# Kernel optimization log

Measured on AMD Instinct MI355X. Metric: run time of the kernel, lower is better.

The kernel has to match this reference:

```python
import jax, jax.numpy as jnp
import numpy as np

D = 1024          # hidden_dim
H = 16            # num_heads
G = 32            # number of graphs in the batch
N = 512           # nodes per graph (equal-size graphs -> the per-graph loop becomes one batched attention)
T = G * N         # total nodes
EPS = 1e-5


def _layernorm(x, g, b):
    mu = jnp.mean(x, axis=-1, keepdims=True)
    var = jnp.mean(jnp.square(x - mu), axis=-1, keepdims=True)
    return (x - mu) * jax.lax.rsqrt(var + EPS) * g + b


def setup_inputs() -> dict:
    key = jax.random.key(0)
    ks = jax.random.split(key, 10)
    s = 0.02
    inp = {
        "h": jax.random.normal(ks[0], (T, D), dtype=jnp.float32),
        "w_in": jax.random.normal(ks[1], (3 * D, D), dtype=jnp.float32) * s,   # MHA in_proj_weight
        "b_in": jnp.zeros((3 * D,), dtype=jnp.float32),
        "w_out": jax.random.normal(ks[2], (D, D), dtype=jnp.float32) * s,      # MHA out_proj
        "b_out": jnp.zeros((D,), dtype=jnp.float32),
        "ln1_g": jnp.ones((D,), dtype=jnp.float32),
        "ln1_b": jnp.zeros((D,), dtype=jnp.float32),
        "ln2_g": jnp.ones((D,), dtype=jnp.float32),
        "ln2_b": jnp.zeros((D,), dtype=jnp.float32),
        "ffn_w1": jax.random.normal(ks[3], (2 * D, D), dtype=jnp.float32) * s,
        "ffn_b1": jnp.zeros((2 * D,), dtype=jnp.float32),
        "ffn_w2": jax.random.normal(ks[4], (D, 2 * D), dtype=jnp.float32) * s,
        "ffn_b2": jnp.zeros((D,), dtype=jnp.float32),
        "edge_index": jax.random.randint(ks[5], (2, 65536), 0, T, dtype=jnp.int64),
        "batch": jnp.repeat(jnp.arange(G, dtype=jnp.int64), N),
        "num_graphs": G,
    }
    return inp


def reference(h, w_in, b_in, w_out, b_out, ln1_g, ln1_b, ln2_g, ln2_b,
              ffn_w1, ffn_b1, ffn_w2, ffn_b2, edge_index, batch, num_graphs):
    # Per-graph self-attention: equal-size contiguous graphs -> reshape to [G, N, D]
    hd = D // H
    x = h.reshape(num_graphs, -1, D)                       # [G, N, D]
    n = x.shape[1]
    qkv = x @ w_in.T + b_in                                # [G, N, 3D]
    q, k, v = jnp.split(qkv, 3, axis=-1)
    q = q.reshape(num_graphs, n, H, hd).transpose(0, 2, 1, 3)  # [G, H, N, hd]
    k = k.reshape(num_graphs, n, H, hd).transpose(0, 2, 1, 3)
    v = v.reshape(num_graphs, n, H, hd).transpose(0, 2, 1, 3)
    scores = jnp.einsum('ghnd,ghmd->ghnm', q, k) / np.sqrt(hd)
    attn = jax.nn.softmax(scores, axis=-1)
    o = jnp.einsum('ghnm,ghmd->ghnd', attn, v)             # [G, H, N, hd]
    o = o.transpose(0, 2, 1, 3).reshape(num_graphs, n, D)
    o = o @ w_out.T + b_out
    x = _layernorm(x + o, ln1_g, ln1_b)                    # residual + norm1
    f = jax.nn.relu(x @ ffn_w1.T + ffn_b1) @ ffn_w2.T + ffn_b2  # dropout: eval mode (identity)
    x = _layernorm(x + f, ln2_g, ln2_b)                    # residual + norm2
    return x.reshape(-1, D)                                # [T, D]
```

## Files before the change

### kernel.cpp

```cpp
#include <hip/hip_runtime.h>
#include <stdint.h>

typedef unsigned short u16;
typedef __attribute__((ext_vector_type(8))) short bf16x8;
typedef __attribute__((ext_vector_type(4))) float f32x4;

#define AS1C(p) ((const __attribute__((address_space(1))) char*)(const char*)(p))
#define AS3C(p) ((__attribute__((address_space(3))) char*)(char*)(p))

static __device__ __forceinline__ u16 f2bf(float f) {
  uint32_t u = __builtin_bit_cast(uint32_t, f);
  u = (u + 0x7FFFu + ((u >> 16) & 1u)) >> 16;
  return (u16)u;
}

__global__ __launch_bounds__(256) void k_f2bf(const float* __restrict__ src,
                                              u16* __restrict__ dst, int n4) {
  int i = blockIdx.x * blockDim.x + threadIdx.x;
  if (i >= n4) return;
  float4 v = reinterpret_cast<const float4*>(src)[i];
  ushort4 o;
  o.x = f2bf(v.x); o.y = f2bf(v.y); o.z = f2bf(v.z); o.w = f2bf(v.w);
  reinterpret_cast<ushort4*>(dst)[i] = o;
}

#define BAR()  do { asm volatile("" ::: "memory"); __builtin_amdgcn_s_barrier(); asm volatile("" ::: "memory"); } while (0)
#define WLG()  asm volatile("s_waitcnt lgkmcnt(0)" ::: "memory")
#define WV4()  asm volatile("s_waitcnt vmcnt(4)" ::: "memory")

template<bool OUT_BF16, bool RELU>
__global__ __launch_bounds__(512, 2) void k_gemm256(const u16* __restrict__ A,
                                                    const u16* __restrict__ B,
                                                    const float* __restrict__ bias,
                                                    void* __restrict__ C,
                                                    int M, int N, int K) {
  __shared__ __align__(16) char lds[131072];
  const int tid = threadIdx.x, lane = tid & 63, wid = tid >> 6;
  const int wm = wid >> 2, wn = wid & 3;

  const int nbx = N >> 8;
  const int cpx = gridDim.x >> 3;
  const int sid = ((int)blockIdx.x & 7) * cpx + ((int)blockIdx.x >> 3);
  const int bm = (sid / nbx) << 8;
  const int bn = (sid % nbx) << 8;

  int ga[2], gb[2];
  unsigned wdst[2];
#pragma unroll
  for (int c = 0; c < 2; ++c) {
    const int o = wid * 2048 + c * 1024 + lane * 16;
    const int r = o >> 7;
    const int kb = (((o >> 4) & 7) ^ (r & 7)) * 16;
    ga[c] = (bm + r) * K * 2 + kb;
    gb[c] = (bn + r) * K * 2 + kb;
    wdst[c] = (unsigned)__builtin_amdgcn_readfirstlane(wid * 2048 + c * 1024);
  }
  const int hStep = 128 * K * 2;
  const char* Ag = (const char*)A;
  const char* Bg = (const char*)B;

  const int rA = (wm * 128 + (lane & 15)) * 128;
  const int rB = 32768 + (wn * 64 + (lane & 15)) * 128;
  int ck[2];
#pragma unroll
  for (int s = 0; s < 2; ++s) ck[s] = ((s * 4 + (lane >> 4)) ^ (lane & 7)) * 16;

  f32x4 acc[8][4];
#pragma unroll
  for (int m = 0; m < 8; ++m)
#pragma unroll
    for (int n = 0; n < 4; ++n) acc[m][n] = 0.f;
  bf16x8 am[4][2], b0f[2][2], b1f[2][2];

#define STG(isB, half, t, buf) do { \
  _Pragma("unroll") for (int c_ = 0; c_ < 2; ++c_) { \
    const char* s_ = ((isB) ? Bg : Ag) + ((isB) ? gb[c_] : ga[c_]) + (half) * hStep + (t) * 128; \
    __builtin_amdgcn_global_load_lds(AS1C(s_), \
        AS3C(lds + ((buf) * 65536 + (isB) * 32768 + (half) * 16384 + wdst[c_])), 16, 0, 0); \
  } } while (0)

#define RDA(buf, mh) do { \
  _Pragma("unroll") for (int m_ = 0; m_ < 4; ++m_) \
  _Pragma("unroll") for (int s_ = 0; s_ < 2; ++s_) \
    am[m_][s_] = *(const bf16x8*)(lds + (buf) * 65536 + rA + ((mh) * 64 + m_ * 16) * 128 + ck[s_]); } while (0)

#define RDB(buf, nh, dst) do { \
  _Pragma("unroll") for (int n_ = 0; n_ < 2; ++n_) \
  _Pragma("unroll") for (int s_ = 0; s_ < 2; ++s_) \
    dst[n_][s_] = *(const bf16x8*)(lds + (buf) * 65536 + rB + ((nh) * 32 + n_ * 16) * 128 + ck[s_]); } while (0)

#define MM(mh, nh, bf) do { \
  __builtin_amdgcn_s_setprio(1); \
  _Pragma("unroll") for (int m_ = 0; m_ < 4; ++m_) \
  _Pragma("unroll") for (int n_ = 0; n_ < 2; ++n_) \
  _Pragma("unroll") for (int s_ = 0; s_ < 2; ++s_) \
    acc[(mh) * 4 + m_][(nh) * 2 + n_] = __builtin_amdgcn_mfma_f32_16x16x32_bf16( \
        am[m_][s_], bf[n_][s_], acc[(mh) * 4 + m_][(nh) * 2 + n_], 0, 0, 0); \
  __builtin_amdgcn_s_setprio(0); } while (0)

  const int nT = K >> 6, tmask = nT - 1, nIter = K >> 7;

  STG(1, 0, 0, 0); STG(1, 1, 0, 0); STG(0, 0, 0, 0); STG(0, 1, 0, 0);
  STG(1, 0, 1, 1); STG(1, 1, 1, 1);
  WV4();
  BAR();

  for (int i = 0; i < nIter; ++i) {
    const int t1 = 2 * i + 1;
    const int t2 = (2 * i + 2) & tmask;
    const int t3 = (2 * i + 3) & tmask;
    RDA(0, 0); RDB(0, 0, b0f); STG(0, 0, t1, 1); BAR(); WLG(); MM(0, 0, b0f); BAR();
    RDB(0, 1, b1f); STG(0, 1, t1, 1); BAR(); WLG(); MM(0, 1, b1f); BAR();
    RDA(0, 1); STG(1, 0, t2, 0); BAR(); WLG(); MM(1, 1, b1f); BAR();
    STG(1, 1, t2, 0); WV4(); BAR(); MM(1, 0, b0f); BAR();
    RDA(1, 0); RDB(1, 0, b0f); STG(0, 0, t2, 0); BAR(); WLG(); MM(0, 0, b0f); BAR();
    RDB(1, 1, b1f); STG(0, 1, t2, 0); BAR(); WLG(); MM(0, 1, b1f); BAR();
    RDA(1, 1); STG(1, 0, t3, 1); BAR(); WLG(); MM(1, 1, b1f); BAR();
    STG(1, 1, t3, 1); WV4(); BAR(); MM(1, 0, b0f); BAR();
  }
  asm volatile("s_waitcnt vmcnt(0)" ::: "memory");

  u16* Cb = (u16*)C;
  float* Cf = (float*)C;
#pragma unroll
  for (int n = 0; n < 4; ++n) {
    const int col = bn + wn * 64 + n * 16 + (lane & 15);
    const float bv = bias[col];
#pragma unroll
    for (int m = 0; m < 8; ++m) {
      const int rbase = bm + wm * 128 + m * 16 + (lane >> 4) * 4;
#pragma unroll
      for (int q = 0; q < 4; ++q) {
        float v = acc[m][n][q] + bv;
        if (RELU) v = fmaxf(v, 0.f);
        const long idx = (long)(rbase + q) * N + col;
        if (OUT_BF16) Cb[idx] = f2bf(v);
        else          Cf[idx] = v;
      }
    }
  }
#undef STG
#undef RDA
#undef RDB
#undef MM
}

__global__ __launch_bounds__(256) void k_transpose_v(const u16* __restrict__ qkv,
                                                     u16* __restrict__ vt) {
  const int gh = blockIdx.x, g = gh >> 4, h = gh & 15;
  const int tid = threadIdx.x;
  __shared__ __align__(16) u16 tile[4096];
  for (int nt = 0; nt < 8; ++nt) {
    const int n0 = nt * 64;
#pragma unroll
    for (int c = 0; c < 2; ++c) {
      const int ch = tid * 2 + c;
      const int n = ch >> 3;
      const int cc = ch & 7;
      const uint4 v = *reinterpret_cast<const uint4*>(
          qkv + (long)(g * 512 + n0 + n) * 3072 + 2048 + h * 64 + cc * 8);
      const int phys = cc ^ (n & 7) ^ (n >> 3);
      *reinterpret_cast<uint4*>(tile + n * 64 + phys * 8) = v;
    }
    __syncthreads();
#pragma unroll
    for (int c = 0; c < 2; ++c) {
      const int ch = tid * 2 + c;
      const int crow = ch >> 3;
      const int noff = (ch & 7) * 8;
      union { u16 s[8]; uint4 u; } val;
#pragma unroll
      for (int i = 0; i < 8; ++i) {
        const int n = noff + i;
        const int phys = (crow >> 3) ^ (n & 7) ^ (n >> 3);
        val.s[i] = tile[n * 64 + phys * 8 + (crow & 7)];
      }
      *reinterpret_cast<uint4*>(vt + (long)(gh * 64 + crow) * 512 + n0 + noff) = val.u;
    }
    __syncthreads();
  }
}

__global__ __launch_bounds__(256) void k_attn(const u16* __restrict__ qkv,
                                              const u16* __restrict__ vt,
                                              u16* __restrict__ out) {
  __shared__ __align__(16) char Ks[8192];
  __shared__ __align__(16) char Vs[8192];
  __shared__ __align__(16) char Ps[4][2048];
  const int tid = threadIdx.x, lane = tid & 63, wid = tid >> 6;
  const int qb = blockIdx.x, h = blockIdx.y, g = blockIdx.z;
  const int gh = g * 16 + h;
  const long grow0 = (long)g * 512;
  const char* qbase = (const char*)qkv;

  const long qrow = qb * 64 + wid * 16 + (lane & 15);
  bf16x8 qf[2];
#pragma unroll
  for (int kf = 0; kf < 2; ++kf) {
    const long go = (((grow0 + qrow) * 3072) + h * 64 + kf * 32 + (lane >> 4) * 8) * 2;
    qf[kf] = *reinterpret_cast<const bf16x8*>(qbase + go);
  }

  f32x4 oacc[4];
#pragma unroll
  for (int i = 0; i < 4; i++) oacc[i] = 0.f;
  float mrun[4], lrun[4];
#pragma unroll
  for (int q = 0; q < 4; q++) { mrun[q] = -3.0e38f; lrun[q] = 0.f; }

  const unsigned l0 = (unsigned)__builtin_amdgcn_readfirstlane(wid * 2048);
  const unsigned l1 = l0 + 1024;

  for (int it = 0; it < 8; ++it) {
    const int kv0 = it * 64;
#pragma unroll
    for (int c = 0; c < 2; ++c) {
      const int o = wid * 2048 + c * 1024 + lane * 16;
      const int row = o >> 7;
      const int pch = (o >> 4) & 7;
      const int lch = pch ^ (row & 7);
      const long gK = (((grow0 + kv0 + row) * 3072) + 1024 + h * 64 + lch * 8) * 2;
      __builtin_amdgcn_global_load_lds(AS1C(qbase + gK), AS3C(Ks + (c ? l1 : l0)), 16, 0, 0);
      const long gV = (((long)(gh * 64 + row)) * 512 + kv0 + lch * 8) * 2;
      __builtin_amdgcn_global_load_lds(AS1C((const char*)vt + gV), AS3C(Vs + (c ? l1 : l0)), 16, 0, 0);
    }
    __syncthreads();

    f32x4 s[4];
#pragma unroll
    for (int nt = 0; nt < 4; ++nt) {
      const int krow = nt * 16 + (lane & 15);
      const int sw = krow & 7;
      const bf16x8 k0 = *reinterpret_cast<const bf16x8*>(Ks + krow * 128 + (((lane >> 4)) ^ sw) * 16);
      const bf16x8 k1 = *reinterpret_cast<const bf16x8*>(Ks + krow * 128 + (((lane >> 4) + 4) ^ sw) * 16);
      f32x4 t = 0.f;
      t = __builtin_amdgcn_mfma_f32_16x16x32_bf16(qf[0], k0, t, 0, 0, 0);
      t = __builtin_amdgcn_mfma_f32_16x16x32_bf16(qf[1], k1, t, 0, 0, 0);
#pragma unroll
      for (int q = 0; q < 4; q++) t[q] *= 0.125f;
      s[nt] = t;
    }

    float tmax[4];
#pragma unroll
    for (int q = 0; q < 4; q++)
      tmax[q] = fmaxf(fmaxf(s[0][q], s[1][q]), fmaxf(s[2][q], s[3][q]));
#pragma unroll
    for (int d = 1; d < 16; d <<= 1)
#pragma unroll
      for (int q = 0; q < 4; q++) tmax[q] = fmaxf(tmax[q], __shfl_xor(tmax[q], d));
    float sf[4];
#pragma unroll
    for (int q = 0; q < 4; q++) {
      const float mn = fmaxf(mrun[q], tmax[q]);
      sf[q] = __expf(mrun[q] - mn);
      mrun[q] = mn;
    }
    float rs[4] = {0.f, 0.f, 0.f, 0.f};
#pragma unroll
    for (int nt = 0; nt < 4; nt++)
#pragma unroll
      for (int q = 0; q < 4; q++) {
        const float p = __expf(s[nt][q] - mrun[q]);
        s[nt][q] = p;
        rs[q] += p;
      }
#pragma unroll
    for (int d = 1; d < 16; d <<= 1)
#pragma unroll
      for (int q = 0; q < 4; q++) rs[q] += __shfl_xor(rs[q], d);
#pragma unroll
    for (int q = 0; q < 4; q++) lrun[q] = lrun[q] * sf[q] + rs[q];
#pragma unroll
    for (int i = 0; i < 4; i++)
#pragma unroll
      for (int q = 0; q < 4; q++) oacc[i][q] *= sf[q];

    char* pw = Ps[wid];
#pragma unroll
    for (int nt = 0; nt < 4; nt++) {
      const int cc = nt * 16 + (lane & 15);
#pragma unroll
      for (int q = 0; q < 4; q++) {
        const int r = (lane >> 4) * 4 + q;
        const int phys = (cc >> 3) ^ (r & 7);
        *(u16*)(pw + r * 128 + phys * 16 + (cc & 7) * 2) = f2bf(s[nt][q]);
      }
    }

#pragma unroll
    for (int kf = 0; kf < 2; ++kf) {
      const int prow = lane & 15;
      const bf16x8 pa = *reinterpret_cast<const bf16x8*>(
          pw + prow * 128 + ((kf * 4 + (lane >> 4)) ^ (prow & 7)) * 16);
#pragma unroll
      for (int ot = 0; ot < 4; ++ot) {
        const int vr = ot * 16 + (lane & 15);
        const bf16x8 vb = *reinterpret_cast<const bf16x8*>(
            Vs + vr * 128 + ((kf * 4 + (lane >> 4)) ^ (vr & 7)) * 16);
        oacc[ot] = __builtin_amdgcn_mfma_f32_16x16x32_bf16(pa, vb, oacc[ot], 0, 0, 0);
      }
    }
    __syncthreads();
  }

#pragma unroll
  for (int ot = 0; ot < 4; ++ot) {
    const int col = h * 64 + ot * 16 + (lane & 15);
#pragma unroll
    for (int q = 0; q < 4; q++) {
      const long r = grow0 + qb * 64 + wid * 16 + (lane >> 4) * 4 + q;
      out[r * 1024 + col] = f2bf(oacc[ot][q] / lrun[q]);
    }
  }
}

template<bool EMIT_BF16>
__global__ __launch_bounds__(256) void k_ln(const float* __restrict__ A,
                                            const float* __restrict__ Bz,
                                            const float* __restrict__ gam,
                                            const float* __restrict__ bet,
                                            float* __restrict__ out_f,
                                            u16* __restrict__ out_b) {
  const int row = blockIdx.x;
  const int tid = threadIdx.x;
  const long base = (long)row * 1024;
  const float4 a = reinterpret_cast<const float4*>(A + base)[tid];
  const float4 b = reinterpret_cast<const float4*>(Bz + base)[tid];
  const float x0 = a.x + b.x, x1 = a.y + b.y, x2 = a.z + b.z, x3 = a.w + b.w;
  float s1 = x0 + x1 + x2 + x3;
  float s2 = x0 * x0 + x1 * x1 + x2 * x2 + x3 * x3;
#pragma unroll
  for (int d = 1; d < 64; d <<= 1) { s1 += __shfl_xor(s1, d); s2 += __shfl_xor(s2, d); }
  __shared__ float red[8];
  const int wid = tid >> 6, lane = tid & 63;
  if (lane == 0) { red[wid] = s1; red[4 + wid] = s2; }
  __syncthreads();
  s1 = red[0] + red[1] + red[2] + red[3];
  s2 = red[4] + red[5] + red[6] + red[7];
  const float mu = s1 * (1.f / 1024.f);
  const float var = s2 * (1.f / 1024.f) - mu * mu;
  const float rstd = rsqrtf(var + 1e-5f);
  const float4 gv = reinterpret_cast<const float4*>(gam)[tid];
  const float4 bv = reinterpret_cast<const float4*>(bet)[tid];
  float4 y;
  y.x = (x0 - mu) * rstd * gv.x + bv.x;
  y.y = (x1 - mu) * rstd * gv.y + bv.y;
  y.z = (x2 - mu) * rstd * gv.z + bv.z;
  y.w = (x3 - mu) * rstd * gv.w + bv.w;
  reinterpret_cast<float4*>(out_f + base)[tid] = y;
  if (EMIT_BF16) {
    ushort4 o;
    o.x = f2bf(y.x); o.y = f2bf(y.y); o.z = f2bf(y.z); o.w = f2bf(y.w);
    reinterpret_cast<ushort4*>(out_b + base)[tid] = o;
  }
}

extern "C" void kernel_launch(void* const* d_in, const int* in_sizes, int n_in,
                              void* d_out, int out_size, void* d_ws, size_t ws_size,
                              hipStream_t stream) {
  const float* h    = (const float*)d_in[0];
  const float* w_in = (const float*)d_in[1];
  const float* b_in = (const float*)d_in[2];
  const float* w_o  = (const float*)d_in[3];
  const float* b_o  = (const float*)d_in[4];
  const float* ln1g = (const float*)d_in[5];
  const float* ln1b = (const float*)d_in[6];
  const float* ln2g = (const float*)d_in[7];
  const float* ln2b = (const float*)d_in[8];
  const float* w1   = (const float*)d_in[9];
  const float* b1   = (const float*)d_in[10];
  const float* w2   = (const float*)d_in[11];
  const float* b2   = (const float*)d_in[12];

  const size_t WS_NEED = 184549376;
  if (ws_size < WS_NEED) {
    hipMemsetAsync(d_out, 0, (size_t)out_size * 4, stream);
    return;
  }

  char* W = (char*)d_ws;
  u16* h_bf     = (u16*)(W + 0);
  u16* w_in_bf  = (u16*)(W + 33554432);
  u16* w_out_bf = (u16*)(W + 39845888);
  u16* w1_bf    = (u16*)(W + 41943040);
  u16* w2_bf    = (u16*)(W + 46137344);
  u16* qkv      = (u16*)(W + 50331648);
  u16* vt       = (u16*)(W + 150994944);
  float* x1     = (float*)(W + 50331648);
  u16* f1       = (u16*)(W + 117440512);
  u16* attn_bf  = h_bf;
  u16* x1_bf    = h_bf;
  float* o32    = (float*)d_out;
  float* f2     = (float*)d_out;

  k_f2bf<<<dim3(16384), 256, 0, stream>>>(h, h_bf, 4194304);
  k_f2bf<<<dim3(3072),  256, 0, stream>>>(w_in, w_in_bf, 786432);
  k_f2bf<<<dim3(1024),  256, 0, stream>>>(w_o, w_out_bf, 262144);
  k_f2bf<<<dim3(2048),  256, 0, stream>>>(w1, w1_bf, 524288);
  k_f2bf<<<dim3(2048),  256, 0, stream>>>(w2, w2_bf, 524288);

  k_gemm256<true, false><<<dim3(768), 512, 0, stream>>>(h_bf, w_in_bf, b_in, (void*)qkv, 16384, 3072, 1024);
  k_transpose_v<<<dim3(512), 256, 0, stream>>>(qkv, vt);
  k_attn<<<dim3(8, 16, 32), 256, 0, stream>>>(qkv, vt, attn_bf);
  k_gemm256<false, false><<<dim3(256), 512, 0, stream>>>(attn_bf, w_out_bf, b_o, (void*)o32, 16384, 1024, 1024);
  k_ln<true><<<dim3(16384), 256, 0, stream>>>(h, o32, ln1g, ln1b, x1, x1_bf);
  k_gemm256<true, true><<<dim3(512), 512, 0, stream>>>(x1_bf, w1_bf, b1, (void*)f1, 16384, 2048, 1024);
  k_gemm256<false, false><<<dim3(256), 512, 0, stream>>>(f1, w2_bf, b2, (void*)f2, 16384, 1024, 2048);
  k_ln<false><<<dim3(16384), 256, 0, stream>>>(x1, f2, ln2g, ln2b, (float*)d_out, (u16*)nullptr);
}
```

Measured before the change: 684.7 us.

## Restructure GEMM mainloop to triple-buffered 32-wide K tiles with one barrier

Replaces the double-buffered 64-wide K tile GEMM pipeline, which used eight phases and many barriers per iteration, with a three-stage ring of 32-wide K tiles. Each step issues all fragment reads, launches the global-to-LDS prefetch two tiles ahead, and splits the MFMAs into two halves gated by partial lgkmcnt waits. There is a single barrier per step. LDS drops from 128KB to 96KB and the swizzle changes to a 4-chunk pattern. This is meant to cut barrier overhead and improve load/compute overlap, at the cost of smaller K steps (more iterations) and a shallower swizzle that may add bank conflicts.

```diff
diff --git a/kernel.cpp b/kernel.cpp
--- a/kernel.cpp
+++ b/kernel.cpp
@@ -24,17 +24,13 @@
   reinterpret_cast<ushort4*>(dst)[i] = o;
 }
 
-#define BAR()  do { asm volatile("" ::: "memory"); __builtin_amdgcn_s_barrier(); asm volatile("" ::: "memory"); } while (0)
-#define WLG()  asm volatile("s_waitcnt lgkmcnt(0)" ::: "memory")
-#define WV4()  asm volatile("s_waitcnt vmcnt(4)" ::: "memory")
-
 template<bool OUT_BF16, bool RELU>
 __global__ __launch_bounds__(512, 2) void k_gemm256(const u16* __restrict__ A,
                                                     const u16* __restrict__ B,
                                                     const float* __restrict__ bias,
                                                     void* __restrict__ C,
                                                     int M, int N, int K) {
-  __shared__ __align__(16) char lds[131072];
+  __shared__ __align__(16) char lds[98304];
   const int tid = threadIdx.x, lane = tid & 63, wid = tid >> 6;
   const int wm = wid >> 2, wn = wid & 3;
 
@@ -49,74 +45,75 @@
 #pragma unroll
   for (int c = 0; c < 2; ++c) {
     const int o = wid * 2048 + c * 1024 + lane * 16;
-    const int r = o >> 7;
-    const int kb = (((o >> 4) & 7) ^ (r & 7)) * 16;
+    const int r = o >> 6;
+    const int kb = (((o >> 4) & 3) ^ (r & 3)) * 16;
     ga[c] = (bm + r) * K * 2 + kb;
     gb[c] = (bn + r) * K * 2 + kb;
     wdst[c] = (unsigned)__builtin_amdgcn_readfirstlane(wid * 2048 + c * 1024);
   }
-  const int hStep = 128 * K * 2;
   const char* Ag = (const char*)A;
   const char* Bg = (const char*)B;
 
-  const int rA = (wm * 128 + (lane & 15)) * 128;
-  const int rB = 32768 + (wn * 64 + (lane & 15)) * 128;
-  int ck[2];
-#pragma unroll
-  for (int s = 0; s < 2; ++s) ck[s] = ((s * 4 + (lane >> 4)) ^ (lane & 7)) * 16;
+  const int arow = wm * 128 + (lane & 15);
+  const int brow = wn * 64 + (lane & 15);
+  const int ckA = ((lane >> 4) ^ (arow & 3)) * 16;
+  const int ckB = ((lane >> 4) ^ (brow & 3)) * 16;
 
   f32x4 acc[8][4];
 #pragma unroll
   for (int m = 0; m < 8; ++m)
 #pragma unroll
     for (int n = 0; n < 4; ++n) acc[m][n] = 0.f;
-  bf16x8 am[4][2], b0f[2][2], b1f[2][2];
-
-#define STG(isB, half, t, buf) do { \
+  bf16x8 am[8], bfr[4];
+
+#define STG(t, b) do { \
+  const int koff_ = (t) * 64; \
   _Pragma("unroll") for (int c_ = 0; c_ < 2; ++c_) { \
-    const char* s_ = ((isB) ? Bg : Ag) + ((isB) ? gb[c_] : ga[c_]) + (half) * hStep + (t) * 128; \
-    __builtin_amdgcn_global_load_lds(AS1C(s_), \
-        AS3C(lds + ((buf) * 65536 + (isB) * 32768 + (half) * 16384 + wdst[c_])), 16, 0, 0); \
+    __builtin_amdgcn_global_load_lds(AS1C(Ag + ga[c_] + koff_), \
+        AS3C(lds + ((b) * 32768 + wdst[c_])), 16, 0, 0); \
+    __builtin_amdgcn_global_load_lds(AS1C(Bg + gb[c_] + koff_), \
+        AS3C(lds + ((b) * 32768 + 16384 + wdst[c_])), 16, 0, 0); \
   } } while (0)
 
-#define RDA(buf, mh) do { \
-  _Pragma("unroll") for (int m_ = 0; m_ < 4; ++m_) \
-  _Pragma("unroll") for (int s_ = 0; s_ < 2; ++s_) \
-    am[m_][s_] = *(const bf16x8*)(lds + (buf) * 65536 + rA + ((mh) * 64 + m_ * 16) * 128 + ck[s_]); } while (0)
-
-#define RDB(buf, nh, dst) do { \
-  _Pragma("unroll") for (int n_ = 0; n_ < 2; ++n_) \
-  _Pragma("unroll") for (int s_ = 0; s_ < 2; ++s_) \
-    dst[n_][s_] = *(const bf16x8*)(lds + (buf) * 65536 + rB + ((nh) * 32 + n_ * 16) * 128 + ck[s_]); } while (0)
-
-#define MM(mh, nh, bf) do { \
+#define MM(mh) do { \
   __builtin_amdgcn_s_setprio(1); \
   _Pragma("unroll") for (int m_ = 0; m_ < 4; ++m_) \
-  _Pragma("unroll") for (int n_ = 0; n_ < 2; ++n_) \
-  _Pragma("unroll") for (int s_ = 0; s_ < 2; ++s_) \
-    acc[(mh) * 4 + m_][(nh) * 2 + n_] = __builtin_amdgcn_mfma_f32_16x16x32_bf16( \
-        am[m_][s_], bf[n_][s_], acc[(mh) * 4 + m_][(nh) * 2 + n_], 0, 0, 0); \
+  _Pragma("unroll") for (int n_ = 0; n_ < 4; ++n_) \
+    acc[(mh) * 4 + m_][n_] = __builtin_amdgcn_mfma_f32_16x16x32_bf16( \
+        am[(mh) * 4 + m_], bfr[n_], acc[(mh) * 4 + m_][n_], 0, 0, 0); \
   __builtin_amdgcn_s_setprio(0); } while (0)
 
-  const int nT = K >> 6, tmask = nT - 1, nIter = K >> 7;
-
-  STG(1, 0, 0, 0); STG(1, 1, 0, 0); STG(0, 0, 0, 0); STG(0, 1, 0, 0);
-  STG(1, 0, 1, 1); STG(1, 1, 1, 1);
-  WV4();
-  BAR();
-
-  for (int i = 0; i < nIter; ++i) {
-    const int t1 = 2 * i + 1;
-    const int t2 = (2 * i + 2) & tmask;
-    const int t3 = (2 * i + 3) & tmask;
-    RDA(0, 0); RDB(0, 0, b0f); STG(0, 0, t1, 1); BAR(); WLG(); MM(0, 0, b0f); BAR();
-    RDB(0, 1, b1f); STG(0, 1, t1, 1); BAR(); WLG(); MM(0, 1, b1f); BAR();
-    RDA(0, 1); STG(1, 0, t2, 0); BAR(); WLG(); MM(1, 1, b1f); BAR();
-    STG(1, 1, t2, 0); WV4(); BAR(); MM(1, 0, b0f); BAR();
-    RDA(1, 0); RDB(1, 0, b0f); STG(0, 0, t2, 0); BAR(); WLG(); MM(0, 0, b0f); BAR();
-    RDB(1, 1, b1f); STG(0, 1, t2, 0); BAR(); WLG(); MM(0, 1, b1f); BAR();
-    RDA(1, 1); STG(1, 0, t3, 1); BAR(); WLG(); MM(1, 1, b1f); BAR();
-    STG(1, 1, t3, 1); WV4(); BAR(); MM(1, 0, b0f); BAR();
+  const int nT = K >> 5, tmask = nT - 1;
+
+  STG(0, 0); STG(1, 1);
+  asm volatile("s_waitcnt vmcnt(4)" ::: "memory");
+  __builtin_amdgcn_sched_barrier(0);
+  __builtin_amdgcn_s_barrier();
+
+  int bR = 0;
+  for (int t = 0; t < nT; ++t) {
+    const int bW = (bR >= 1) ? bR - 1 : 2;
+    const int base = bR * 32768;
+#pragma unroll
+    for (int m_ = 0; m_ < 4; ++m_)
+      am[m_] = *(const bf16x8*)(lds + base + (arow + m_ * 16) * 64 + ckA);
+#pragma unroll
+    for (int n_ = 0; n_ < 4; ++n_)
+      bfr[n_] = *(const bf16x8*)(lds + base + 16384 + (brow + n_ * 16) * 64 + ckB);
+#pragma unroll
+    for (int m_ = 4; m_ < 8; ++m_)
+      am[m_] = *(const bf16x8*)(lds + base + (arow + m_ * 16) * 64 + ckA);
+    STG((t + 2) & tmask, bW);
+    asm volatile("s_waitcnt lgkmcnt(4)" ::: "memory");
+    __builtin_amdgcn_sched_barrier(0);
+    MM(0);
+    asm volatile("s_waitcnt lgkmcnt(0)" ::: "memory");
+    __builtin_amdgcn_sched_barrier(0);
+    MM(1);
+    asm volatile("s_waitcnt vmcnt(4)" ::: "memory");
+    __builtin_amdgcn_sched_barrier(0);
+    __builtin_amdgcn_s_barrier();
+    bR = (bR == 2) ? 0 : bR + 1;
   }
   asm volatile("s_waitcnt vmcnt(0)" ::: "memory");
 
@@ -140,8 +137,6 @@
     }
   }
 #undef STG
-#undef RDA
-#undef RDB
 #undef MM
 }
 
```

Result: no change. 685.1 us (+0.1%).
